# Performance work log

Hardware: AMD Instinct MI355X
Metric: run time of the kernel (lower is better)

## Reference

```python
import jax, jax.numpy as jnp
import numpy as np
import math

D_MODEL = 1024
N_HEADS = 16
HEAD_DIM = D_MODEL // N_HEADS
PAD_INDEX = 0
NEG_INF = -1e9  # matches torch masked_fill value


def setup_inputs() -> dict:
    key = jax.random.key(0)
    ks = jax.random.split(key, 10)
    b, s = 2, 2048
    x = jax.random.normal(ks[0], (b, s, D_MODEL), dtype=jnp.float32)
    input_ids = jax.random.randint(ks[1], (b, s), 0, 32000, dtype=jnp.int64)
    scale = 1.0 / math.sqrt(D_MODEL)
    def lin(k):
        kw, kb = jax.random.split(k)
        W = jax.random.uniform(kw, (D_MODEL, D_MODEL), jnp.float32, -scale, scale)
        bb = jax.random.uniform(kb, (D_MODEL,), jnp.float32, -scale, scale)
        return W, bb
    Wq, bq = lin(ks[2])
    Wk, bk = lin(ks[3])
    Wv, bv = lin(ks[4])
    Wo, bo = lin(ks[5])
    return {"x": x, "input_ids": input_ids,
            "Wq": Wq, "bq": bq, "Wk": Wk, "bk": bk,
            "Wv": Wv, "bv": bv, "Wo": Wo, "bo": bo}


def reference(x, input_ids, Wq, bq, Wk, bk, Wv, bv, Wo, bo):
    b, s, _ = x.shape
    # torch nn.Linear: y = x @ W.T + b
    q = (x @ Wq.T + bq).reshape(b, s, N_HEADS, HEAD_DIM)
    k = (x @ Wk.T + bk).reshape(b, s, N_HEADS, HEAD_DIM)
    v = (x @ Wv.T + bv).reshape(b, s, N_HEADS, HEAD_DIM)
    # scores: [b, h, s, s]
    scores = jnp.einsum('bqhd,bkhd->bhqk', q, k) / math.sqrt(HEAD_DIM)
    pad_mask = (input_ids != PAD_INDEX)[:, None, None, :]          # [b,1,1,s] over keys
    causal = jnp.tril(jnp.ones((s, s), dtype=bool))[None, None]     # [1,1,s,s]
    final_mask = pad_mask & causal
    scores = jnp.where(final_mask, scores, NEG_INF)
    attn = jax.nn.softmax(scores, axis=-1)
    out = jnp.einsum('bhqk,bkhd->bqhd', attn, v).reshape(b, s, D_MODEL)
    return out @ Wo.T + bo
```

## Files before the change

kernel.cpp:

```cpp
#include <hip/hip_runtime.h>

#define DMODEL 1024
#define NHEADS 16
#define HDIM   64
#define BATCH  2
#define SEQ    2048
#define MROWS  (BATCH*SEQ)

typedef __bf16 bf16x8 __attribute__((ext_vector_type(8)));
typedef __bf16 bf16x4 __attribute__((ext_vector_type(4)));
typedef float floatx4 __attribute__((ext_vector_type(4)));

typedef const __attribute__((address_space(1))) void gvoid;
typedef __attribute__((address_space(3))) void lvoid;

template<bool V> struct ICb { static constexpr bool value = V; };

#define QSCALE 0.18033688011112042f

__global__ void cast_all(const float* __restrict__ x,
                         const float* __restrict__ wq, const float* __restrict__ wk,
                         const float* __restrict__ wv, const float* __restrict__ wo,
                         __bf16* __restrict__ xb, __bf16* __restrict__ wqb,
                         __bf16* __restrict__ wkb, __bf16* __restrict__ wvb,
                         __bf16* __restrict__ wob)
{
  const int i = blockIdx.x * 256 + threadIdx.x;
  const float* s; __bf16* o; int off;
  if (i < MROWS*DMODEL/4) { s = x; o = xb; off = i; }
  else {
    const int r = i - MROWS*DMODEL/4;
    const int w = r >> 18;
    off = r & 262143;
    s = (w == 0) ? wq : (w == 1) ? wk : (w == 2) ? wv : wo;
    o = (w == 0) ? wqb : (w == 1) ? wkb : (w == 2) ? wvb : wob;
  }
  const float4 f = ((const float4*)s)[off];
  bf16x4 v = {(__bf16)f.x, (__bf16)f.y, (__bf16)f.z, (__bf16)f.w};
  *(bf16x4*)(o + off*4) = v;
}

template<int MODE>
__global__ __launch_bounds__(256, 3)
void gemm_nt(const unsigned short* __restrict__ A,
             const unsigned short* __restrict__ W0,
             const unsigned short* __restrict__ W1,
             const unsigned short* __restrict__ W2,
             const float* __restrict__ b0,
             const float* __restrict__ b1,
             const float* __restrict__ b2,
             unsigned short* __restrict__ qout,
             unsigned short* __restrict__ kout,
             unsigned short* __restrict__ vout,
             float* __restrict__ outf)
{
  const int K = DMODEL;
  __shared__ unsigned short As[2][128*32];
  __shared__ unsigned short Bs[2][128*32];
  const int tid  = threadIdx.x;
  const int wid  = tid >> 6;
  const int lane = tid & 63;

  const int lin = blockIdx.x;
  const int wg  = (MODE == 0) ? ((lin & 7)*96 + (lin >> 3))
                              : ((lin & 7)*32 + (lin >> 3));
  const int bx  = (MODE == 0) ? (wg % 24) : (wg & 7);
  const int by  = (MODE == 0) ? (wg / 24) : (wg >> 3);
  const int brow = by * 128;
  const int bcol = bx * 128;
  const int wr = (wid >> 1) * 64;
  const int wc = (wid & 1) * 64;

  int which = 0;
  const unsigned short* Bw = W0;
  const float* bias = b0;
  int bcolL = bcol;
  if (MODE == 0) {
    which = bcol >> 10;
    Bw   = which == 0 ? W0 : which == 1 ? W1 : W2;
    bias = which == 0 ? b0 : which == 1 ? b1 : b2;
    bcolL = bcol & 1023;
  }

  floatx4 acc[4][4] = {};

  const int sr = wid*16 + (lane >> 2);
  const int sc = (lane & 3) * 8;
  const int fr = lane & 15;
  const int fk = (lane >> 4) * 8;

#define GSTAGE(KT, B) do {                                                     \
    _Pragma("unroll")                                                          \
    for (int i_ = 0; i_ < 2; ++i_) {                                           \
      __builtin_amdgcn_global_load_lds(                                        \
          (gvoid*)(A + (size_t)(brow + i_*64 + sr)*K + (KT) + sc),             \
          (lvoid*)(As[B] + i_*2048 + wid*512), 16, 0, 0);                      \
      __builtin_amdgcn_global_load_lds(                                        \
          (gvoid*)(Bw + (size_t)(bcolL + i_*64 + sr)*K + (KT) + sc),           \
          (lvoid*)(Bs[B] + i_*2048 + wid*512), 16, 0, 0);                      \
    }                                                                          \
  } while (0)

  GSTAGE(0, 0);

  for (int kt = 0; kt < K; kt += 32) {
    const int cur = (kt >> 5) & 1;
    if (kt + 32 < K) {
      GSTAGE(kt + 32, cur ^ 1);
      asm volatile("s_waitcnt vmcnt(4)" ::: "memory");
    } else {
      asm volatile("s_waitcnt vmcnt(0)" ::: "memory");
    }
    __builtin_amdgcn_s_barrier();
    __builtin_amdgcn_sched_barrier(0);

    bf16x8 af[4], bfv[4];
#pragma unroll
    for (int m = 0; m < 4; ++m)
      af[m] = *(const bf16x8*)(As[cur] + (wr + m*16 + fr)*32 + fk);
#pragma unroll
    for (int n = 0; n < 4; ++n)
      bfv[n] = *(const bf16x8*)(Bs[cur] + (wc + n*16 + fr)*32 + fk);
    __builtin_amdgcn_s_setprio(1);
#pragma unroll
    for (int m = 0; m < 4; ++m)
#pragma unroll
      for (int n = 0; n < 4; ++n)
        acc[m][n] = __builtin_amdgcn_mfma_f32_16x16x32_bf16(af[m], bfv[n], acc[m][n], 0, 0, 0);
    __builtin_amdgcn_s_setprio(0);
    __builtin_amdgcn_s_barrier();
  }
#undef GSTAGE

  const int er = (lane >> 4) * 4;
  const int ec = lane & 15;
#pragma unroll
  for (int m = 0; m < 4; ++m) {
#pragma unroll
    for (int n = 0; n < 4; ++n) {
      const int colL = bcolL + wc + n*16 + ec;
      const float bv = bias[colL];
      const int rowb = brow + wr + m*16 + er;
      if (MODE == 0) {
        const int bi = rowb >> 11, s = rowb & 2047;
        const int hh = colL >> 6, dd = colL & 63;
        if (which == 2) {
          bf16x4 v4 = {(__bf16)(acc[m][n][0] + bv), (__bf16)(acc[m][n][1] + bv),
                       (__bf16)(acc[m][n][2] + bv), (__bf16)(acc[m][n][3] + bv)};
          *(bf16x4*)((__bf16*)vout + ((size_t)(bi*NHEADS + hh)*HDIM + dd)*SEQ + s) = v4;
        } else if (which == 0) {
          __bf16* o = (__bf16*)qout;
#pragma unroll
          for (int j = 0; j < 4; ++j)
            o[((size_t)(bi*NHEADS + hh)*SEQ + s + j)*HDIM + dd] =
                (__bf16)((acc[m][n][j] + bv) * QSCALE);
        } else {
          __bf16* o = (__bf16*)kout;
#pragma unroll
          for (int j = 0; j < 4; ++j)
            o[((size_t)(bi*NHEADS + hh)*SEQ + s + j)*HDIM + dd] = (__bf16)(acc[m][n][j] + bv);
        }
      } else {
#pragma unroll
        for (int j = 0; j < 4; ++j)
          outf[(size_t)(rowb + j)*DMODEL + colL] = acc[m][n][j] + bv;
      }
    }
  }
}

__global__ __launch_bounds__(256, 4)
void attn_fwd(const unsigned short* __restrict__ qb,
              const unsigned short* __restrict__ kb,
              const unsigned short* __restrict__ vtb,
              const int* __restrict__ ids,
              unsigned short* __restrict__ outb)
{
  const int hb = blockIdx.x;
  const int h = hb & 15, bi = hb >> 4;
  const int y = blockIdx.y;
  const int jm = y >> 3, mm = y & 7;
  const int qt = jm*8 + ((jm & 1) ? 7 - mm : mm);

  const int tid = threadIdx.x, wid = tid >> 6, lane = tid & 63;
  const int qbase = qt * 64;
  const size_t hoff = (size_t)(bi*NHEADS + h) * SEQ * HDIM;
  const unsigned short* Qh  = qb  + hoff;
  const unsigned short* Kh  = kb  + hoff;
  const unsigned short* Vth = vtb + hoff;

  __shared__ unsigned short Ks[2][64*64];
  __shared__ unsigned short Vs[2][64*64];
  __shared__ unsigned short Ps[4][16*64];

  const int q_   = lane & 15;
  const int hi4  = lane >> 4;
  const int koff = hi4 * 4;
  const int qg = qbase + wid*16 + q_;

  bf16x8 qf[2];
#pragma unroll
  for (int c = 0; c < 2; ++c)
    qf[c] = *(const bf16x8*)(Qh + (size_t)qg*HDIM + c*32 + hi4*8);

  const int r0 = tid >> 3;
  const int sw = ((tid & 7) ^ (r0 & 7)) * 8;
  unsigned short* Pw = Ps[wid];

#define STAGE(T, B) do {                                                       \
    const unsigned short* kbase_ = Kh + (size_t)((T)*64) * HDIM;               \
    const unsigned short* vbase_ = Vth + (T)*64;                               \
    __builtin_amdgcn_global_load_lds((gvoid*)(kbase_ + r0*64 + sw),            \
                                     (lvoid*)(Ks[B] + tid*8), 16, 0, 0);       \
    __builtin_amdgcn_global_load_lds((gvoid*)(kbase_ + (r0+32)*64 + sw),       \
                                     (lvoid*)(Ks[B] + (tid+256)*8), 16, 0, 0); \
    __builtin_amdgcn_global_load_lds((gvoid*)(vbase_ + (size_t)r0*SEQ + sw),   \
                                     (lvoid*)(Vs[B] + tid*8), 16, 0, 0);       \
    __builtin_amdgcn_global_load_lds((gvoid*)(vbase_ + (size_t)(r0+32)*SEQ + sw),\
                                     (lvoid*)(Vs[B] + (tid+256)*8), 16, 0, 0); \
  } while (0)

  float lsum = 0.f;
  floatx4 Oacc[4] = {};

  auto step = [&](auto Mc, int kb0, int bufc, unsigned long long wm) {
    constexpr bool MASKED = decltype(Mc)::value;

    floatx4 st[4];
    __builtin_amdgcn_s_setprio(1);
#pragma unroll
    for (int t = 0; t < 4; ++t) {
      st[t] = (floatx4){0.f, 0.f, 0.f, 0.f};
      const int kr = t*16 + q_;
#pragma unroll
      for (int c = 0; c < 2; ++c) {
        const int cd = ((c*4 + hi4) ^ (kr & 7)) * 8;
        bf16x8 kf = *(const bf16x8*)(Ks[bufc] + kr*64 + cd);
        st[t] = __builtin_amdgcn_mfma_f32_16x16x32_bf16(kf, qf[c], st[t], 0, 0, 0);
      }
    }
    __builtin_amdgcn_s_setprio(0);

    float ps = 0.f;
#pragma unroll
    for (int t = 0; t < 4; ++t) {
      float p[4];
#pragma unroll
      for (int r = 0; r < 4; ++r) {
        float pv = exp2f(st[t][r]);
        if (MASKED) {
          const int ko = t*16 + koff + r;
          const bool dead = ((kb0 + ko) > qg) || (((wm >> ko) & 1ull) != 0ull);
          pv = dead ? 0.f : pv;
        }
        p[r] = pv;
        ps += pv;
      }
      bf16x4 pk = {(__bf16)p[0], (__bf16)p[1], (__bf16)p[2], (__bf16)p[3]};
      const int ko = t*16 + koff;
      *(bf16x4*)(Pw + q_*64 + (((ko >> 3) ^ (q_ & 7)) * 8) + (ko & 7)) = pk;
    }
    lsum += ps;

    __builtin_amdgcn_s_setprio(1);
#pragma unroll
    for (int cp = 0; cp < 2; ++cp) {
      const int ko = cp*32 + hi4*8;
      bf16x8 pf = *(const bf16x8*)(Pw + q_*64 + (((ko >> 3) ^ (q_ & 7)) * 8));
#pragma unroll
      for (int n = 0; n < 4; ++n) {
        const int d = n*16 + q_;
        const int cd = ((cp*4 + hi4) ^ (d & 7)) * 8;
        bf16x8 vf = *(const bf16x8*)(Vs[bufc] + d*64 + cd);
        Oacc[n] = __builtin_amdgcn_mfma_f32_16x16x32_bf16(pf, vf, Oacc[n], 0, 0, 0);
      }
    }
    __builtin_amdgcn_s_setprio(0);
  };

  const int nT = qt + 1;
  STAGE(0, 0);

  for (int kbv = 0; kbv < nT; ++kbv) {
    const int kb0 = kbv * 64;
    const int bufc = kbv & 1;
    const bool last = (kbv == nT - 1);
    const int pv = ids[bi*SEQ + kb0 + lane];
    if (!last) {
      STAGE(kbv + 1, bufc ^ 1);
      asm volatile("s_waitcnt vmcnt(4)" ::: "memory");
    } else {
      asm volatile("s_waitcnt vmcnt(0)" ::: "memory");
    }
    const unsigned long long wm = __ballot(pv == 0);
    __builtin_amdgcn_s_barrier();
    __builtin_amdgcn_sched_barrier(0);

    if (!last && wm == 0ull) step(ICb<false>{}, kb0, bufc, 0ull);
    else                     step(ICb<true >{}, kb0, bufc, wm);
    __builtin_amdgcn_s_barrier();
  }
#undef STAGE

  float lt = lsum + __shfl_xor(lsum, 16);
  lt += __shfl_xor(lt, 32);

#pragma unroll
  for (int r = 0; r < 4; ++r) {
    const float inv = 1.f / __shfl(lt, koff + r);
    const int row = bi*SEQ + qbase + wid*16 + koff + r;
#pragma unroll
    for (int n = 0; n < 4; ++n)
      ((__bf16*)outb)[(size_t)row*DMODEL + h*HDIM + n*16 + q_] = (__bf16)(Oacc[n][r] * inv);
  }
}

extern "C" void kernel_launch(void* const* d_in, const int* in_sizes, int n_in,
                              void* d_out, int out_size, void* d_ws, size_t ws_size,
                              hipStream_t stream)
{
  const float* x  = (const float*)d_in[0];
  const int*   ids= (const int*)d_in[1];
  const float* Wq = (const float*)d_in[2];
  const float* bq = (const float*)d_in[3];
  const float* Wk = (const float*)d_in[4];
  const float* bk = (const float*)d_in[5];
  const float* Wv = (const float*)d_in[6];
  const float* bv = (const float*)d_in[7];
  const float* Wo = (const float*)d_in[8];
  const float* bo = (const float*)d_in[9];
  float* out = (float*)d_out;

  char* ws = (char*)d_ws;
  unsigned short* xb   = (unsigned short*)(ws);
  unsigned short* wqb  = (unsigned short*)(ws + ( 8u<<20));
  unsigned short* wkb  = (unsigned short*)(ws + (10u<<20));
  unsigned short* wvb  = (unsigned short*)(ws + (12u<<20));
  unsigned short* wob  = (unsigned short*)(ws + (14u<<20));
  unsigned short* qbuf = (unsigned short*)(ws + (16u<<20));
  unsigned short* kbuf = (unsigned short*)(ws + (24u<<20));
  unsigned short* vbuf = (unsigned short*)(ws + (32u<<20));
  unsigned short* abuf = (unsigned short*)(ws + (40u<<20));

  cast_all<<<8192, 256, 0, stream>>>(x, Wq, Wk, Wv, Wo,
                                     (__bf16*)xb, (__bf16*)wqb, (__bf16*)wkb,
                                     (__bf16*)wvb, (__bf16*)wob);

  gemm_nt<0><<<768, 256, 0, stream>>>(xb, wqb, wkb, wvb, bq, bk, bv,
                                      qbuf, kbuf, vbuf, nullptr);

  attn_fwd<<<dim3(32, 32), 256, 0, stream>>>(qbuf, kbuf, vbuf, ids, abuf);

  gemm_nt<1><<<256, 256, 0, stream>>>(abuf, wob, wob, wob, bo, bo, bo,
                                      nullptr, nullptr, nullptr, out);
}
```

Baseline: 116.8 us.

## Split attention KV loop across two wave groups and merge partial results

Attention blocks now use 512 threads split into two groups of four waves. Each group processes half of the causal key tiles for the same 64 query rows, with its own double-buffered K/V LDS stages. The partial outputs and row sums are combined through shared memory at the end. The grid becomes 1D and is ordered longest-query-tile-first, to improve load balance. The trade-off is double the LDS footprint, an extra reduction and barrier at the end, and lower occupancy per CU.

```diff
diff --git a/kernel.cpp b/kernel.cpp
--- a/kernel.cpp
+++ b/kernel.cpp
@@ -169,55 +169,59 @@
   }
 }
 
-__global__ __launch_bounds__(256, 4)
+__global__ __launch_bounds__(512, 4)
 void attn_fwd(const unsigned short* __restrict__ qb,
               const unsigned short* __restrict__ kb,
               const unsigned short* __restrict__ vtb,
               const int* __restrict__ ids,
               unsigned short* __restrict__ outb)
 {
-  const int hb = blockIdx.x;
+  const int bx = blockIdx.x;
+  const int hb = bx & 31;
+  const int qt = 31 - (bx >> 5);
   const int h = hb & 15, bi = hb >> 4;
-  const int y = blockIdx.y;
-  const int jm = y >> 3, mm = y & 7;
-  const int qt = jm*8 + ((jm & 1) ? 7 - mm : mm);
 
   const int tid = threadIdx.x, wid = tid >> 6, lane = tid & 63;
+  const int grp  = wid >> 2;
+  const int wid4 = wid & 3;
   const int qbase = qt * 64;
   const size_t hoff = (size_t)(bi*NHEADS + h) * SEQ * HDIM;
   const unsigned short* Qh  = qb  + hoff;
   const unsigned short* Kh  = kb  + hoff;
   const unsigned short* Vth = vtb + hoff;
 
-  __shared__ unsigned short Ks[2][64*64];
-  __shared__ unsigned short Vs[2][64*64];
-  __shared__ unsigned short Ps[4][16*64];
+  __shared__ unsigned short Ks[2][2][64*64];
+  __shared__ unsigned short Vs[2][2][64*64];
+  __shared__ unsigned short Ps[8][16*64];
+  float* LOf = (float*)Ps;
+  float* Ll  = (float*)Ks;
 
   const int q_   = lane & 15;
   const int hi4  = lane >> 4;
   const int koff = hi4 * 4;
-  const int qg = qbase + wid*16 + q_;
+  const int qg = qbase + wid4*16 + q_;
 
   bf16x8 qf[2];
 #pragma unroll
   for (int c = 0; c < 2; ++c)
     qf[c] = *(const bf16x8*)(Qh + (size_t)qg*HDIM + c*32 + hi4*8);
 
-  const int r0 = tid >> 3;
-  const int sw = ((tid & 7) ^ (r0 & 7)) * 8;
+  const int gt = tid & 255;
+  const int r0 = gt >> 3;
+  const int sw = ((gt & 7) ^ (r0 & 7)) * 8;
   unsigned short* Pw = Ps[wid];
 
 #define STAGE(T, B) do {                                                       \
     const unsigned short* kbase_ = Kh + (size_t)((T)*64) * HDIM;               \
     const unsigned short* vbase_ = Vth + (T)*64;                               \
     __builtin_amdgcn_global_load_lds((gvoid*)(kbase_ + r0*64 + sw),            \
-                                     (lvoid*)(Ks[B] + tid*8), 16, 0, 0);       \
+                                     (lvoid*)(Ks[grp][B] + gt*8), 16, 0, 0);   \
     __builtin_amdgcn_global_load_lds((gvoid*)(kbase_ + (r0+32)*64 + sw),       \
-                                     (lvoid*)(Ks[B] + (tid+256)*8), 16, 0, 0); \
+                                     (lvoid*)(Ks[grp][B] + (gt+256)*8), 16, 0, 0);\
     __builtin_amdgcn_global_load_lds((gvoid*)(vbase_ + (size_t)r0*SEQ + sw),   \
-                                     (lvoid*)(Vs[B] + tid*8), 16, 0, 0);       \
+                                     (lvoid*)(Vs[grp][B] + gt*8), 16, 0, 0);   \
     __builtin_amdgcn_global_load_lds((gvoid*)(vbase_ + (size_t)(r0+32)*SEQ + sw),\
-                                     (lvoid*)(Vs[B] + (tid+256)*8), 16, 0, 0); \
+                                     (lvoid*)(Vs[grp][B] + (gt+256)*8), 16, 0, 0);\
   } while (0)
 
   float lsum = 0.f;
@@ -235,7 +239,7 @@
 #pragma unroll
       for (int c = 0; c < 2; ++c) {
         const int cd = ((c*4 + hi4) ^ (kr & 7)) * 8;
-        bf16x8 kf = *(const bf16x8*)(Ks[bufc] + kr*64 + cd);
+        bf16x8 kf = *(const bf16x8*)(Ks[grp][bufc] + kr*64 + cd);
         st[t] = __builtin_amdgcn_mfma_f32_16x16x32_bf16(kf, qf[c], st[t], 0, 0, 0);
       }
     }
@@ -271,7 +275,7 @@
       for (int n = 0; n < 4; ++n) {
         const int d = n*16 + q_;
         const int cd = ((cp*4 + hi4) ^ (d & 7)) * 8;
-        bf16x8 vf = *(const bf16x8*)(Vs[bufc] + d*64 + cd);
+        bf16x8 vf = *(const bf16x8*)(Vs[grp][bufc] + d*64 + cd);
         Oacc[n] = __builtin_amdgcn_mfma_f32_16x16x32_bf16(pf, vf, Oacc[n], 0, 0, 0);
       }
     }
@@ -279,15 +283,21 @@
   };
 
   const int nT = qt + 1;
-  STAGE(0, 0);
-
-  for (int kbv = 0; kbv < nT; ++kbv) {
-    const int kb0 = kbv * 64;
-    const int bufc = kbv & 1;
-    const bool last = (kbv == nT - 1);
-    const int pv = ids[bi*SEQ + kb0 + lane];
-    if (!last) {
-      STAGE(kbv + 1, bufc ^ 1);
+  const int h0 = (nT + 1) >> 1;
+  const int cnt = (grp == 0) ? h0 : nT - h0;
+  const int tb  = (grp == 0) ? 0 : h0;
+  const int H = h0;
+
+  if (cnt > 0) STAGE(tb, 0);
+
+  for (int i = 0; i < H; ++i) {
+    const bool valid = (i < cnt);
+    const int t = tb + i;
+    const int kb0 = t * 64;
+    int pv = 1;
+    if (valid) pv = ids[bi*SEQ + kb0 + lane];
+    if (i + 1 < cnt) {
+      STAGE(t + 1, (i + 1) & 1);
       asm volatile("s_waitcnt vmcnt(4)" ::: "memory");
     } else {
       asm volatile("s_waitcnt vmcnt(0)" ::: "memory");
@@ -296,8 +306,11 @@
     __builtin_amdgcn_s_barrier();
     __builtin_amdgcn_sched_barrier(0);
 
-    if (!last && wm == 0ull) step(ICb<false>{}, kb0, bufc, 0ull);
-    else                     step(ICb<true >{}, kb0, bufc, wm);
+    if (valid) {
+      const int bufc = i & 1;
+      if ((t != nT - 1) && wm == 0ull) step(ICb<false>{}, kb0, bufc, 0ull);
+      else                             step(ICb<true >{}, kb0, bufc, wm);
+    }
     __builtin_amdgcn_s_barrier();
   }
 #undef STAGE
@@ -305,13 +318,27 @@
   float lt = lsum + __shfl_xor(lsum, 16);
   lt += __shfl_xor(lt, 32);
 
-#pragma unroll
-  for (int r = 0; r < 4; ++r) {
-    const float inv = 1.f / __shfl(lt, koff + r);
-    const int row = bi*SEQ + qbase + wid*16 + koff + r;
-#pragma unroll
-    for (int n = 0; n < 4; ++n)
-      ((__bf16*)outb)[(size_t)row*DMODEL + h*HDIM + n*16 + q_] = (__bf16)(Oacc[n][r] * inv);
+  if (grp == 1) {
+#pragma unroll
+    for (int r = 0; r < 4; ++r)
+#pragma unroll
+      for (int n = 0; n < 4; ++n)
+        LOf[(wid4*16 + koff + r)*64 + n*16 + q_] = Oacc[n][r];
+    if (hi4 == 0) Ll[wid4*16 + q_] = lt;
+  }
+  __syncthreads();
+  if (grp == 0) {
+#pragma unroll
+    for (int r = 0; r < 4; ++r) {
+      const int rloc = wid4*16 + koff + r;
+      const float inv = 1.f / (__shfl(lt, koff + r) + Ll[rloc]);
+      const int row = bi*SEQ + qbase + rloc;
+#pragma unroll
+      for (int n = 0; n < 4; ++n) {
+        const float o = Oacc[n][r] + LOf[rloc*64 + n*16 + q_];
+        ((__bf16*)outb)[(size_t)row*DMODEL + h*HDIM + n*16 + q_] = (__bf16)(o * inv);
+      }
+    }
   }
 }
 
@@ -349,7 +376,7 @@
   gemm_nt<0><<<768, 256, 0, stream>>>(xb, wqb, wkb, wvb, bq, bk, bv,
                                       qbuf, kbuf, vbuf, nullptr);
 
-  attn_fwd<<<dim3(32, 32), 256, 0, stream>>>(qbuf, kbuf, vbuf, ids, abuf);
+  attn_fwd<<<1024, 512, 0, stream>>>(qbuf, kbuf, vbuf, ids, abuf);
 
   gemm_nt<1><<<256, 256, 0, stream>>>(abuf, wob, wob, wob, bo, bo, bo,
                                       nullptr, nullptr, nullptr, out);
```

Result: faster. 111.6 us, median of 2 (-4.4%).

## Drop LDS staging of K/V tiles and read fragments directly from global

Applied to the files above, without the earlier changes.

Removes the double-buffered K and V shared-memory tiles, their async global-to-LDS staging and the block-wide barriers. Each wave now loads its K and V MFMA fragments straight from global memory, relying on L1/L2 to absorb the reuse across the four waves. The occupancy hint in launch bounds drops from 4 to 2 blocks. This removes barrier sync and LDS traffic, but loses the prefetch overlap, issues redundant global loads per wave, and makes the V reads strided.

```diff
diff --git a/kernel.cpp b/kernel.cpp
--- a/kernel.cpp
+++ b/kernel.cpp
@@ -169,7 +169,7 @@
   }
 }
 
-__global__ __launch_bounds__(256, 4)
+__global__ __launch_bounds__(256, 2)
 void attn_fwd(const unsigned short* __restrict__ qb,
               const unsigned short* __restrict__ kb,
               const unsigned short* __restrict__ vtb,
@@ -189,8 +189,6 @@
   const unsigned short* Kh  = kb  + hoff;
   const unsigned short* Vth = vtb + hoff;
 
-  __shared__ unsigned short Ks[2][64*64];
-  __shared__ unsigned short Vs[2][64*64];
   __shared__ unsigned short Ps[4][16*64];
 
   const int q_   = lane & 15;
@@ -203,27 +201,11 @@
   for (int c = 0; c < 2; ++c)
     qf[c] = *(const bf16x8*)(Qh + (size_t)qg*HDIM + c*32 + hi4*8);
 
-  const int r0 = tid >> 3;
-  const int sw = ((tid & 7) ^ (r0 & 7)) * 8;
   unsigned short* Pw = Ps[wid];
-
-#define STAGE(T, B) do {                                                       \
-    const unsigned short* kbase_ = Kh + (size_t)((T)*64) * HDIM;               \
-    const unsigned short* vbase_ = Vth + (T)*64;                               \
-    __builtin_amdgcn_global_load_lds((gvoid*)(kbase_ + r0*64 + sw),            \
-                                     (lvoid*)(Ks[B] + tid*8), 16, 0, 0);       \
-    __builtin_amdgcn_global_load_lds((gvoid*)(kbase_ + (r0+32)*64 + sw),       \
-                                     (lvoid*)(Ks[B] + (tid+256)*8), 16, 0, 0); \
-    __builtin_amdgcn_global_load_lds((gvoid*)(vbase_ + (size_t)r0*SEQ + sw),   \
-                                     (lvoid*)(Vs[B] + tid*8), 16, 0, 0);       \
-    __builtin_amdgcn_global_load_lds((gvoid*)(vbase_ + (size_t)(r0+32)*SEQ + sw),\
-                                     (lvoid*)(Vs[B] + (tid+256)*8), 16, 0, 0); \
-  } while (0)
-
   float lsum = 0.f;
   floatx4 Oacc[4] = {};
 
-  auto step = [&](auto Mc, int kb0, int bufc, unsigned long long wm) {
+  auto step = [&](auto Mc, int kb0, unsigned long long wm) {
     constexpr bool MASKED = decltype(Mc)::value;
 
     floatx4 st[4];
@@ -231,11 +213,10 @@
 #pragma unroll
     for (int t = 0; t < 4; ++t) {
       st[t] = (floatx4){0.f, 0.f, 0.f, 0.f};
-      const int kr = t*16 + q_;
+      const int kr = kb0 + t*16 + q_;
 #pragma unroll
       for (int c = 0; c < 2; ++c) {
-        const int cd = ((c*4 + hi4) ^ (kr & 7)) * 8;
-        bf16x8 kf = *(const bf16x8*)(Ks[bufc] + kr*64 + cd);
+        bf16x8 kf = *(const bf16x8*)(Kh + (size_t)kr*HDIM + c*32 + hi4*8);
         st[t] = __builtin_amdgcn_mfma_f32_16x16x32_bf16(kf, qf[c], st[t], 0, 0, 0);
       }
     }
@@ -270,37 +251,19 @@
 #pragma unroll
       for (int n = 0; n < 4; ++n) {
         const int d = n*16 + q_;
-        const int cd = ((cp*4 + hi4) ^ (d & 7)) * 8;
-        bf16x8 vf = *(const bf16x8*)(Vs[bufc] + d*64 + cd);
+        bf16x8 vf = *(const bf16x8*)(Vth + (size_t)d*SEQ + kb0 + cp*32 + hi4*8);
         Oacc[n] = __builtin_amdgcn_mfma_f32_16x16x32_bf16(pf, vf, Oacc[n], 0, 0, 0);
       }
     }
     __builtin_amdgcn_s_setprio(0);
   };
 
-  const int nT = qt + 1;
-  STAGE(0, 0);
-
-  for (int kbv = 0; kbv < nT; ++kbv) {
+  for (int kbv = 0; kbv <= qt; ++kbv) {
     const int kb0 = kbv * 64;
-    const int bufc = kbv & 1;
-    const bool last = (kbv == nT - 1);
-    const int pv = ids[bi*SEQ + kb0 + lane];
-    if (!last) {
-      STAGE(kbv + 1, bufc ^ 1);
-      asm volatile("s_waitcnt vmcnt(4)" ::: "memory");
-    } else {
-      asm volatile("s_waitcnt vmcnt(0)" ::: "memory");
-    }
-    const unsigned long long wm = __ballot(pv == 0);
-    __builtin_amdgcn_s_barrier();
-    __builtin_amdgcn_sched_barrier(0);
-
-    if (!last && wm == 0ull) step(ICb<false>{}, kb0, bufc, 0ull);
-    else                     step(ICb<true >{}, kb0, bufc, wm);
-    __builtin_amdgcn_s_barrier();
-  }
-#undef STAGE
+    const unsigned long long wm = __ballot(ids[bi*SEQ + kb0 + lane] == 0);
+    if ((kbv != qt) && wm == 0ull) step(ICb<false>{}, kb0, 0ull);
+    else                           step(ICb<true >{}, kb0, wm);
+  }
 
   float lt = lsum + __shfl_xor(lsum, 16);
   lt += __shfl_xor(lt, 32);
```

Result: slower. 189.6 us (+62.3%).
